# Performance work log

Measured on AMD Instinct MI355X. Metric: run time of the kernel, lower is better.

The kernel has to match this reference:

```python
import jax, jax.numpy as jnp
import numpy as np

N_NODES = 100000
N_EDGES = 1000000
D_IN = 128
D_OUT = 128
ALPHA = 0.5


def setup_inputs() -> dict:
    key = jax.random.key(0)
    k = jax.random.split(key, 8)
    x = jax.random.normal(k[0], (N_NODES, D_IN), dtype=jnp.float32)
    edge_src = jax.random.randint(k[1], (N_EDGES,), 0, N_NODES, dtype=jnp.int32)
    edge_dst = jax.random.randint(k[2], (N_EDGES,), 0, N_NODES, dtype=jnp.int32)
    s = 1.0 / np.sqrt(D_IN)
    W_sd = jax.random.uniform(k[3], (D_OUT, D_IN), jnp.float32, -s, s)
    b_sd = jax.random.uniform(k[4], (D_OUT,), jnp.float32, -s, s)
    W_ds = jax.random.uniform(k[5], (D_OUT, D_IN), jnp.float32, -s, s)
    b_ds = jax.random.uniform(k[6], (D_OUT,), jnp.float32, -s, s)
    return {"x": x, "edge_src": edge_src, "edge_dst": edge_dst,
            "W_sd": W_sd, "b_sd": b_sd, "W_ds": W_ds, "b_ds": b_ds}


def reference(x, edge_src, edge_dst, W_sd, b_sd, W_ds, b_ds):
    # adj[dst, src] = 1 for each edge.
    # adj @ x      : aggregate source features into destination rows.
    # adj.T @ x    : aggregate destination features into source rows.
    agg_sd = jax.ops.segment_sum(x[edge_src], edge_dst, num_segments=N_NODES)  # [N, D_IN]
    agg_ds = jax.ops.segment_sum(x[edge_dst], edge_src, num_segments=N_NODES)  # [N, D_IN]
    src_to_dst = agg_sd @ W_sd.T + b_sd  # torch Linear: x W^T + b
    dst_to_src = agg_ds @ W_ds.T + b_ds
    return ALPHA * src_to_dst + (1.0 - ALPHA) * dst_to_src
```

## Files before the change

kernel.cpp:

```cpp
#include <hip/hip_runtime.h>

#define NN 100000
#define NE 1000000
#define D 128
#define ALPHA 0.5f

#define OFF_W2     102400000UL
#define OFF_CNT    102531072UL
#define OFF_START  102931072UL
#define OFF_CUR    103331072UL
#define OFF_CURSOR 103731072UL
#define OFF_BUF    103731328UL
#define OFF_REC    111731328UL
#define WS_OLD     (OFF_BUF + (size_t)2 * NE * 4)
#define WS_NEW     (OFF_REC + (size_t)2 * NE * 4)

#define NB  391
#define EPB 2048

__global__ __launch_bounds__(256) void build_w2(const float* __restrict__ Wsd,
                                                const float* __restrict__ Wds,
                                                float* __restrict__ W2) {
    int idx = blockIdx.x * 256 + threadIdx.x;
    int k = idx >> 8;
    int j = idx & 255;
    float v;
    if (j < 128) v = ALPHA * Wsd[j * D + k];
    else         v = (1.0f - ALPHA) * Wds[(j - 128) * D + k];
    W2[idx] = v;
}

__global__ __launch_bounds__(256) void transform(const float* __restrict__ x,
                                                 const float* __restrict__ W2,
                                                 float* __restrict__ y) {
    __shared__ float As[64][132];
    const int tid  = threadIdx.x;
    const int brow = blockIdx.x * 64;
    const int bcol = blockIdx.y * 64;

#pragma unroll
    for (int i = 0; i < 8; ++i) {
        int f   = tid + i * 256;
        int row = f >> 5;
        int kc  = (f & 31) << 2;
        float4 g = make_float4(0.f, 0.f, 0.f, 0.f);
        int grow = brow + row;
        if (grow < NN) g = *(const float4*)&x[(size_t)grow * D + kc];
        *(float4*)&As[row][kc] = g;
    }
    __syncthreads();

    const int ty = tid >> 4;
    const int tx = tid & 15;
    float acc[4][4];
#pragma unroll
    for (int i = 0; i < 4; ++i)
#pragma unroll
        for (int j = 0; j < 4; ++j) acc[i][j] = 0.f;

#pragma unroll 2
    for (int k0 = 0; k0 < 128; k0 += 4) {
        float av[4][4], bv[4][4];
#pragma unroll
        for (int i = 0; i < 4; ++i) {
            float4 t = *(const float4*)&As[ty * 4 + i][k0];
            av[i][0] = t.x; av[i][1] = t.y; av[i][2] = t.z; av[i][3] = t.w;
        }
#pragma unroll
        for (int j = 0; j < 4; ++j) {
            float4 t = *(const float4*)&W2[(size_t)(k0 + j) * 256 + bcol + tx * 4];
            bv[j][0] = t.x; bv[j][1] = t.y; bv[j][2] = t.z; bv[j][3] = t.w;
        }
#pragma unroll
        for (int i = 0; i < 4; ++i)
#pragma unroll
            for (int c = 0; c < 4; ++c)
#pragma unroll
                for (int kk = 0; kk < 4; ++kk)
                    acc[i][c] += av[i][kk] * bv[kk][c];
    }

#pragma unroll
    for (int i = 0; i < 4; ++i) {
        int row = brow + ty * 4 + i;
        if (row < NN) {
            float4 v = make_float4(acc[i][0], acc[i][1], acc[i][2], acc[i][3]);
            *(float4*)&y[(size_t)row * 256 + bcol + tx * 4] = v;
        }
    }
}

__global__ __launch_bounds__(512) void zero_bins(int* __restrict__ binCnt) {
    int i = threadIdx.x;
    if (i < NB) binCnt[i] = 0;
}

__global__ __launch_bounds__(256) void count_bins(const int* __restrict__ esrc,
                                                  const int* __restrict__ edst,
                                                  int* __restrict__ binCnt) {
    __shared__ int h[NB];
    int t = threadIdx.x;
    for (int i = t; i < NB; i += 256) h[i] = 0;
    __syncthreads();
    int e0 = blockIdx.x * EPB;
    for (int i = t; i < EPB; i += 256) {
        int e = e0 + i;
        if (e < NE) {
            atomicAdd(&h[edst[e] >> 8], 1);
            atomicAdd(&h[esrc[e] >> 8], 1);
        }
    }
    __syncthreads();
    for (int i = t; i < NB; i += 256)
        if (h[i]) atomicAdd(&binCnt[i], h[i]);
}

__global__ __launch_bounds__(256) void scan_bins(const int* __restrict__ binCnt,
                                                 int* __restrict__ binBase,
                                                 int* __restrict__ binCursor) {
    __shared__ int v[NB];
    int t = threadIdx.x;
    for (int i = t; i < NB; i += 256) v[i] = binCnt[i];
    __syncthreads();
    if (t == 0) {
        int acc = 0;
        for (int i = 0; i < NB; ++i) { int c = v[i]; v[i] = acc; acc += c; }
    }
    __syncthreads();
    for (int i = t; i < NB; i += 256) { binBase[i] = v[i]; binCursor[i] = v[i]; }
}

__global__ __launch_bounds__(256) void place_bins(const int* __restrict__ esrc,
                                                  const int* __restrict__ edst,
                                                  int* __restrict__ binCursor,
                                                  int* __restrict__ rec4) {
    __shared__ int h[NB];
    __shared__ int base[NB];
    __shared__ int lcur[NB];
    int t = threadIdx.x;
    for (int i = t; i < NB; i += 256) h[i] = 0;
    __syncthreads();
    int e0 = blockIdx.x * EPB;
    for (int i = t; i < EPB; i += 256) {
        int e = e0 + i;
        if (e < NE) {
            atomicAdd(&h[edst[e] >> 8], 1);
            atomicAdd(&h[esrc[e] >> 8], 1);
        }
    }
    __syncthreads();
    for (int i = t; i < NB; i += 256) {
        if (h[i]) base[i] = atomicAdd(&binCursor[i], h[i]);
        lcur[i] = 0;
    }
    __syncthreads();
    for (int i = t; i < EPB; i += 256) {
        int e = e0 + i;
        if (e < NE) {
            int s = esrc[e], d = edst[e];
            int bd = d >> 8, bs = s >> 8;
            int p1 = atomicAdd(&lcur[bd], 1);
            rec4[base[bd] + p1] = ((d & 255) << 18) | (s << 1);
            int p2 = atomicAdd(&lcur[bs], 1);
            rec4[base[bs] + p2] = ((s & 255) << 18) | (d << 1) | 1;
        }
    }
}

__global__ __launch_bounds__(256) void build_csr(const int* __restrict__ rec4,
                                                 const int* __restrict__ binBase,
                                                 const int* __restrict__ binCnt,
                                                 int* __restrict__ buf,
                                                 int* __restrict__ start,
                                                 int* __restrict__ cnt_out) {
    __shared__ int hc[256];
    __shared__ int st[256];
    int b = blockIdx.x;
    int t = threadIdx.x;
    int node0 = b << 8;
    int r0 = binBase[b];
    int rn = binCnt[b];

    hc[t] = 0;
    __syncthreads();
    for (int i = t; i < rn; i += 256)
        atomicAdd(&hc[rec4[r0 + i] >> 18], 1);
    __syncthreads();
    if (t == 0) {
        int acc = 0;
        for (int i = 0; i < 256; ++i) { st[i] = acc; acc += hc[i]; }
    }
    __syncthreads();
    int n = node0 + t;
    if (n < NN) {
        start[n]   = r0 + st[t];
        cnt_out[n] = hc[t];
    }
    hc[t] = st[t];
    __syncthreads();
    for (int i = t; i < rn; i += 256) {
        int r = rec4[r0 + i];
        int pos = atomicAdd(&hc[r >> 18], 1);
        buf[r0 + pos] = (r & 0x3FFFF) << 7;
    }
}

__global__ __launch_bounds__(256) void gather(const int* __restrict__ start,
                                              const int* __restrict__ cnt,
                                              const int* __restrict__ buf,
                                              const float* __restrict__ y,
                                              const float* __restrict__ bsd,
                                              const float* __restrict__ bds,
                                              float* __restrict__ out) {
    int wave = blockIdx.x * 4 + (threadIdx.x >> 6);
    int lane = threadIdx.x & 63;
    if (wave >= NN) return;
    const int n  = wave;
    const int s0 = start[n];
    const int e0 = s0 + cnt[n];
    const int l2 = lane << 1;

    float a0 = ALPHA * bsd[l2]     + (1.0f - ALPHA) * bds[l2];
    float a1 = ALPHA * bsd[l2 + 1] + (1.0f - ALPHA) * bds[l2 + 1];

    int i = s0;
    for (; i + 4 <= e0; i += 4) {
        int v0 = buf[i], v1 = buf[i + 1], v2 = buf[i + 2], v3 = buf[i + 3];
        float2 p0 = *(const float2*)&y[(size_t)v0 + l2];
        float2 p1 = *(const float2*)&y[(size_t)v1 + l2];
        float2 p2 = *(const float2*)&y[(size_t)v2 + l2];
        float2 p3 = *(const float2*)&y[(size_t)v3 + l2];
        a0 += p0.x + p1.x + p2.x + p3.x;
        a1 += p0.y + p1.y + p2.y + p3.y;
    }
    for (; i < e0; ++i) {
        int v0 = buf[i];
        float2 p0 = *(const float2*)&y[(size_t)v0 + l2];
        a0 += p0.x;
        a1 += p0.y;
    }
    *(float2*)&out[(size_t)n * D + l2] = make_float2(a0, a1);
}

__global__ __launch_bounds__(256) void zero_cnt(int* __restrict__ cnt,
                                                int* __restrict__ cursor) {
    int i = blockIdx.x * 256 + threadIdx.x;
    if (i < NN) cnt[i] = 0;
    if (i == 0) *cursor = 0;
}

__global__ __launch_bounds__(256) void hist(const int* __restrict__ esrc,
                                            const int* __restrict__ edst,
                                            int* __restrict__ cnt) {
    int e = blockIdx.x * 256 + threadIdx.x;
    if (e < NE) {
        atomicAdd(&cnt[edst[e]], 1);
        atomicAdd(&cnt[esrc[e]], 1);
    }
}

__global__ __launch_bounds__(256) void alloc_ranges(const int* __restrict__ cnt,
                                                    int* __restrict__ start,
                                                    int* __restrict__ cur,
                                                    int* __restrict__ cursor) {
    int n    = blockIdx.x * 256 + threadIdx.x;
    int lane = threadIdx.x & 63;
    int v    = (n < NN) ? cnt[n] : 0;
    int incl = v;
#pragma unroll
    for (int off = 1; off < 64; off <<= 1) {
        int t = __shfl_up(incl, off, 64);
        if (lane >= off) incl += t;
    }
    int total = __shfl(incl, 63, 64);
    int base  = 0;
    if (lane == 63) base = atomicAdd(cursor, total);
    base = __shfl(base, 63, 64);
    if (n < NN) {
        int s = base + incl - v;
        start[n] = s;
        cur[n]   = s;
    }
}

__global__ __launch_bounds__(256) void fill(const int* __restrict__ esrc,
                                            const int* __restrict__ edst,
                                            int* __restrict__ cur,
                                            int* __restrict__ buf) {
    int e = blockIdx.x * 256 + threadIdx.x;
    if (e < NE) {
        int s = esrc[e], d = edst[e];
        int p = atomicAdd(&cur[d], 1);
        buf[p] = s * 256;
        int q = atomicAdd(&cur[s], 1);
        buf[q] = d * 256 + 128;
    }
}

__global__ __launch_bounds__(256) void init_out(const float* __restrict__ bsd,
                                                const float* __restrict__ bds,
                                                float* __restrict__ out) {
    int idx = blockIdx.x * 256 + threadIdx.x;
    int d4 = (idx & 31) << 2;
    float4 v;
    v.x = ALPHA * bsd[d4 + 0] + (1.0f - ALPHA) * bds[d4 + 0];
    v.y = ALPHA * bsd[d4 + 1] + (1.0f - ALPHA) * bds[d4 + 1];
    v.z = ALPHA * bsd[d4 + 2] + (1.0f - ALPHA) * bds[d4 + 2];
    v.w = ALPHA * bsd[d4 + 3] + (1.0f - ALPHA) * bds[d4 + 3];
    ((float4*)out)[idx] = v;
}

__global__ __launch_bounds__(256) void scatter(const int* __restrict__ esrc,
                                               const int* __restrict__ edst,
                                               const float* __restrict__ y,
                                               float* __restrict__ out) {
    const int lane = threadIdx.x & 63;
    const int wave = blockIdx.x * 4 + (threadIdx.x >> 6);
    const int nw   = gridDim.x * 4;
    const int l2   = lane << 1;
    for (int e = wave; e < NE; e += nw) {
        int s = esrc[e];
        int d = edst[e];
        float2 a = *(const float2*)&y[(size_t)s * 256 + l2];
        float2 b = *(const float2*)&y[(size_t)d * 256 + 128 + l2];
        float* od = &out[(size_t)d * D + l2];
        float* os = &out[(size_t)s * D + l2];
        unsafeAtomicAdd(od + 0, a.x);
        unsafeAtomicAdd(od + 1, a.y);
        unsafeAtomicAdd(os + 0, b.x);
        unsafeAtomicAdd(os + 1, b.y);
    }
}

extern "C" void kernel_launch(void* const* d_in, const int* in_sizes, int n_in,
                              void* d_out, int out_size, void* d_ws, size_t ws_size,
                              hipStream_t stream) {
    const float* x    = (const float*)d_in[0];
    const int*   esrc = (const int*)  d_in[1];
    const int*   edst = (const int*)  d_in[2];
    const float* Wsd  = (const float*)d_in[3];
    const float* bsd  = (const float*)d_in[4];
    const float* Wds  = (const float*)d_in[5];
    const float* bds  = (const float*)d_in[6];
    float* out = (float*)d_out;

    char* ws = (char*)d_ws;
    float* y  = (float*)ws;
    float* W2 = (float*)(ws + OFF_W2);

    build_w2<<<128, 256, 0, stream>>>(Wsd, Wds, W2);
    transform<<<dim3((NN + 63) / 64, 4), 256, 0, stream>>>(x, W2, y);

    int* cnt    = (int*)(ws + OFF_CNT);
    int* start  = (int*)(ws + OFF_START);
    int* buf    = (int*)(ws + OFF_BUF);

    if (ws_size >= WS_NEW) {
        int* binCnt    = (int*)(ws + OFF_CUR);
        int* binBase   = (int*)(ws + OFF_CUR + 4096);
        int* binCursor = (int*)(ws + OFF_CUR + 8192);
        int* rec4      = (int*)(ws + OFF_REC);
        const int nblk = (NE + EPB - 1) / EPB;
        zero_bins<<<1, 512, 0, stream>>>(binCnt);
        count_bins<<<nblk, 256, 0, stream>>>(esrc, edst, binCnt);
        scan_bins<<<1, 256, 0, stream>>>(binCnt, binBase, binCursor);
        place_bins<<<nblk, 256, 0, stream>>>(esrc, edst, binCursor, rec4);
        build_csr<<<NB, 256, 0, stream>>>(rec4, binBase, binCnt, buf, start, cnt);
        gather<<<(NN + 3) / 4, 256, 0, stream>>>(start, cnt, buf, y, bsd, bds, out);
    } else if (ws_size >= WS_OLD) {
        int* cur    = (int*)(ws + OFF_CUR);
        int* cursor = (int*)(ws + OFF_CURSOR);
        zero_cnt<<<(NN + 255) / 256, 256, 0, stream>>>(cnt, cursor);
        hist<<<(NE + 255) / 256, 256, 0, stream>>>(esrc, edst, cnt);
        alloc_ranges<<<(NN + 255) / 256, 256, 0, stream>>>(cnt, start, cur, cursor);
        fill<<<(NE + 255) / 256, 256, 0, stream>>>(esrc, edst, cur, buf);
        gather<<<(NN + 3) / 4, 256, 0, stream>>>(start, cnt, buf, y, bsd, bds, out);
    } else {
        init_out<<<(NN * D / 4) / 256, 256, 0, stream>>>(bsd, bds, out);
        scatter<<<2048, 256, 0, stream>>>(esrc, edst, y, out);
    }
}
```

Baseline: 419.1 us.

## Aggregate raw features first, then apply a fused K=256 linear transform

Swaps the order of aggregation and linear projection. Each node's incoming and outgoing neighbour features from x are gathered into a 256-wide buffer z, split by edge direction. A single GEMM with a stacked 256x128 weight and a pre-combined bias then produces the output. The gather now reads the smaller x rows instead of the 256-wide transformed y, which is meant to improve cache locality. The GEMM now reads z straight from global memory with no shared-memory staging, and the old fallback paths for smaller workspaces are removed.

```diff
diff --git a/kernel.cpp b/kernel.cpp
--- a/kernel.cpp
+++ b/kernel.cpp
@@ -6,88 +6,32 @@
 #define ALPHA 0.5f
 
 #define OFF_W2     102400000UL
-#define OFF_CNT    102531072UL
-#define OFF_START  102931072UL
-#define OFF_CUR    103331072UL
-#define OFF_CURSOR 103731072UL
-#define OFF_BUF    103731328UL
-#define OFF_REC    111731328UL
-#define WS_OLD     (OFF_BUF + (size_t)2 * NE * 4)
-#define WS_NEW     (OFF_REC + (size_t)2 * NE * 4)
+#define OFF_BIAS   102531072UL
+#define OFF_CNT    102531584UL
+#define OFF_START  102931584UL
+#define OFF_BINC   103331584UL
+#define OFF_BINB   103333632UL
+#define OFF_BINCUR 103335680UL
+#define OFF_BUF    103337728UL
+#define OFF_REC    111337728UL
 
 #define NB  391
 #define EPB 2048
 
-__global__ __launch_bounds__(256) void build_w2(const float* __restrict__ Wsd,
-                                                const float* __restrict__ Wds,
-                                                float* __restrict__ W2) {
+__global__ __launch_bounds__(256) void build_w2b(const float* __restrict__ Wsd,
+                                                 const float* __restrict__ Wds,
+                                                 const float* __restrict__ bsd,
+                                                 const float* __restrict__ bds,
+                                                 float* __restrict__ W2,
+                                                 float* __restrict__ bias) {
     int idx = blockIdx.x * 256 + threadIdx.x;
-    int k = idx >> 8;
-    int j = idx & 255;
+    int k = idx >> 7;
+    int j = idx & 127;
     float v;
-    if (j < 128) v = ALPHA * Wsd[j * D + k];
-    else         v = (1.0f - ALPHA) * Wds[(j - 128) * D + k];
+    if (k < 128) v = ALPHA * Wsd[j * D + k];
+    else         v = (1.0f - ALPHA) * Wds[j * D + (k - 128)];
     W2[idx] = v;
-}
-
-__global__ __launch_bounds__(256) void transform(const float* __restrict__ x,
-                                                 const float* __restrict__ W2,
-                                                 float* __restrict__ y) {
-    __shared__ float As[64][132];
-    const int tid  = threadIdx.x;
-    const int brow = blockIdx.x * 64;
-    const int bcol = blockIdx.y * 64;
-
-#pragma unroll
-    for (int i = 0; i < 8; ++i) {
-        int f   = tid + i * 256;
-        int row = f >> 5;
-        int kc  = (f & 31) << 2;
-        float4 g = make_float4(0.f, 0.f, 0.f, 0.f);
-        int grow = brow + row;
-        if (grow < NN) g = *(const float4*)&x[(size_t)grow * D + kc];
-        *(float4*)&As[row][kc] = g;
-    }
-    __syncthreads();
-
-    const int ty = tid >> 4;
-    const int tx = tid & 15;
-    float acc[4][4];
-#pragma unroll
-    for (int i = 0; i < 4; ++i)
-#pragma unroll
-        for (int j = 0; j < 4; ++j) acc[i][j] = 0.f;
-
-#pragma unroll 2
-    for (int k0 = 0; k0 < 128; k0 += 4) {
-        float av[4][4], bv[4][4];
-#pragma unroll
-        for (int i = 0; i < 4; ++i) {
-            float4 t = *(const float4*)&As[ty * 4 + i][k0];
-            av[i][0] = t.x; av[i][1] = t.y; av[i][2] = t.z; av[i][3] = t.w;
-        }
-#pragma unroll
-        for (int j = 0; j < 4; ++j) {
-            float4 t = *(const float4*)&W2[(size_t)(k0 + j) * 256 + bcol + tx * 4];
-            bv[j][0] = t.x; bv[j][1] = t.y; bv[j][2] = t.z; bv[j][3] = t.w;
-        }
-#pragma unroll
-        for (int i = 0; i < 4; ++i)
-#pragma unroll
-            for (int c = 0; c < 4; ++c)
-#pragma unroll
-                for (int kk = 0; kk < 4; ++kk)
-                    acc[i][c] += av[i][kk] * bv[kk][c];
-    }
-
-#pragma unroll
-    for (int i = 0; i < 4; ++i) {
-        int row = brow + ty * 4 + i;
-        if (row < NN) {
-            float4 v = make_float4(acc[i][0], acc[i][1], acc[i][2], acc[i][3]);
-            *(float4*)&y[(size_t)row * 256 + bcol + tx * 4] = v;
-        }
-    }
+    if (idx < 128) bias[idx] = ALPHA * bsd[idx] + (1.0f - ALPHA) * bds[idx];
 }
 
 __global__ __launch_bounds__(512) void zero_bins(int* __restrict__ binCnt) {
@@ -201,134 +145,108 @@
     for (int i = t; i < rn; i += 256) {
         int r = rec4[r0 + i];
         int pos = atomicAdd(&hc[r >> 18], 1);
-        buf[r0 + pos] = (r & 0x3FFFF) << 7;
-    }
-}
-
-__global__ __launch_bounds__(256) void gather(const int* __restrict__ start,
-                                              const int* __restrict__ cnt,
-                                              const int* __restrict__ buf,
-                                              const float* __restrict__ y,
-                                              const float* __restrict__ bsd,
-                                              const float* __restrict__ bds,
-                                              float* __restrict__ out) {
+        buf[r0 + pos] = r & 0x3FFFF;
+    }
+}
+
+__global__ __launch_bounds__(256) void gather_z(const int* __restrict__ start,
+                                                const int* __restrict__ cnt,
+                                                const int* __restrict__ buf,
+                                                const float* __restrict__ x,
+                                                float* __restrict__ z) {
     int wave = blockIdx.x * 4 + (threadIdx.x >> 6);
     int lane = threadIdx.x & 63;
     if (wave >= NN) return;
-    const int n  = wave;
-    const int s0 = start[n];
-    const int e0 = s0 + cnt[n];
+    const int s0 = start[wave];
+    const int e0 = s0 + cnt[wave];
     const int l2 = lane << 1;
 
-    float a0 = ALPHA * bsd[l2]     + (1.0f - ALPHA) * bds[l2];
-    float a1 = ALPHA * bsd[l2 + 1] + (1.0f - ALPHA) * bds[l2 + 1];
+    float a0 = 0.f, a1 = 0.f;
+    float b0 = 0.f, b1 = 0.f;
+
+#define ACCUM(v, p) if ((v) & 1) { b0 += (p).x; b1 += (p).y; } \
+                    else         { a0 += (p).x; a1 += (p).y; }
 
     int i = s0;
     for (; i + 4 <= e0; i += 4) {
         int v0 = buf[i], v1 = buf[i + 1], v2 = buf[i + 2], v3 = buf[i + 3];
-        float2 p0 = *(const float2*)&y[(size_t)v0 + l2];
-        float2 p1 = *(const float2*)&y[(size_t)v1 + l2];
-        float2 p2 = *(const float2*)&y[(size_t)v2 + l2];
-        float2 p3 = *(const float2*)&y[(size_t)v3 + l2];
-        a0 += p0.x + p1.x + p2.x + p3.x;
-        a1 += p0.y + p1.y + p2.y + p3.y;
+        float2 p0 = *(const float2*)&x[(size_t)(v0 >> 1) * D + l2];
+        float2 p1 = *(const float2*)&x[(size_t)(v1 >> 1) * D + l2];
+        float2 p2 = *(const float2*)&x[(size_t)(v2 >> 1) * D + l2];
+        float2 p3 = *(const float2*)&x[(size_t)(v3 >> 1) * D + l2];
+        ACCUM(v0, p0) ACCUM(v1, p1) ACCUM(v2, p2) ACCUM(v3, p3)
     }
     for (; i < e0; ++i) {
         int v0 = buf[i];
-        float2 p0 = *(const float2*)&y[(size_t)v0 + l2];
-        a0 += p0.x;
-        a1 += p0.y;
-    }
-    *(float2*)&out[(size_t)n * D + l2] = make_float2(a0, a1);
-}
-
-__global__ __launch_bounds__(256) void zero_cnt(int* __restrict__ cnt,
-                                                int* __restrict__ cursor) {
-    int i = blockIdx.x * 256 + threadIdx.x;
-    if (i < NN) cnt[i] = 0;
-    if (i == 0) *cursor = 0;
-}
-
-__global__ __launch_bounds__(256) void hist(const int* __restrict__ esrc,
-                                            const int* __restrict__ edst,
-                                            int* __restrict__ cnt) {
-    int e = blockIdx.x * 256 + threadIdx.x;
-    if (e < NE) {
-        atomicAdd(&cnt[edst[e]], 1);
-        atomicAdd(&cnt[esrc[e]], 1);
-    }
-}
-
-__global__ __launch_bounds__(256) void alloc_ranges(const int* __restrict__ cnt,
-                                                    int* __restrict__ start,
-                                                    int* __restrict__ cur,
-                                                    int* __restrict__ cursor) {
-    int n    = blockIdx.x * 256 + threadIdx.x;
-    int lane = threadIdx.x & 63;
-    int v    = (n < NN) ? cnt[n] : 0;
-    int incl = v;
-#pragma unroll
-    for (int off = 1; off < 64; off <<= 1) {
-        int t = __shfl_up(incl, off, 64);
-        if (lane >= off) incl += t;
-    }
-    int total = __shfl(incl, 63, 64);
-    int base  = 0;
-    if (lane == 63) base = atomicAdd(cursor, total);
-    base = __shfl(base, 63, 64);
-    if (n < NN) {
-        int s = base + incl - v;
-        start[n] = s;
-        cur[n]   = s;
-    }
-}
-
-__global__ __launch_bounds__(256) void fill(const int* __restrict__ esrc,
-                                            const int* __restrict__ edst,
-                                            int* __restrict__ cur,
-                                            int* __restrict__ buf) {
-    int e = blockIdx.x * 256 + threadIdx.x;
-    if (e < NE) {
-        int s = esrc[e], d = edst[e];
-        int p = atomicAdd(&cur[d], 1);
-        buf[p] = s * 256;
-        int q = atomicAdd(&cur[s], 1);
-        buf[q] = d * 256 + 128;
-    }
-}
-
-__global__ __launch_bounds__(256) void init_out(const float* __restrict__ bsd,
-                                                const float* __restrict__ bds,
-                                                float* __restrict__ out) {
-    int idx = blockIdx.x * 256 + threadIdx.x;
-    int d4 = (idx & 31) << 2;
-    float4 v;
-    v.x = ALPHA * bsd[d4 + 0] + (1.0f - ALPHA) * bds[d4 + 0];
-    v.y = ALPHA * bsd[d4 + 1] + (1.0f - ALPHA) * bds[d4 + 1];
-    v.z = ALPHA * bsd[d4 + 2] + (1.0f - ALPHA) * bds[d4 + 2];
-    v.w = ALPHA * bsd[d4 + 3] + (1.0f - ALPHA) * bds[d4 + 3];
-    ((float4*)out)[idx] = v;
-}
-
-__global__ __launch_bounds__(256) void scatter(const int* __restrict__ esrc,
-                                               const int* __restrict__ edst,
-                                               const float* __restrict__ y,
-                                               float* __restrict__ out) {
-    const int lane = threadIdx.x & 63;
-    const int wave = blockIdx.x * 4 + (threadIdx.x >> 6);
-    const int nw   = gridDim.x * 4;
-    const int l2   = lane << 1;
-    for (int e = wave; e < NE; e += nw) {
-        int s = esrc[e];
-        int d = edst[e];
-        float2 a = *(const float2*)&y[(size_t)s * 256 + l2];
-        float2 b = *(const float2*)&y[(size_t)d * 256 + 128 + l2];
-        float* od = &out[(size_t)d * D + l2];
-        float* os = &out[(size_t)s * D + l2];
-        unsafeAtomicAdd(od + 0, a.x);
-        unsafeAtomicAdd(od + 1, a.y);
-        unsafeAtomicAdd(os + 0, b.x);
-        unsafeAtomicAdd(os + 1, b.y);
+        float2 p0 = *(const float2*)&x[(size_t)(v0 >> 1) * D + l2];
+        ACCUM(v0, p0)
+    }
+#undef ACCUM
+
+    *(float2*)&z[(size_t)wave * 256 + l2]       = make_float2(a0, a1);
+    *(float2*)&z[(size_t)wave * 256 + 128 + l2] = make_float2(b0, b1);
+}
+
+__global__ __launch_bounds__(256) void transform_z(const float* __restrict__ z,
+                                                   const float* __restrict__ W2,
+                                                   const float* __restrict__ bias,
+                                                   float* __restrict__ out) {
+    const int tid  = threadIdx.x;
+    const int brow = blockIdx.x * 64;
+    const int ty   = tid >> 4;
+    const int tx   = tid & 15;
+    const int c0   = tx << 2;
+
+    float acc[4][2][4];
+#pragma unroll
+    for (int i = 0; i < 4; ++i)
+#pragma unroll
+        for (int g = 0; g < 2; ++g)
+#pragma unroll
+            for (int c = 0; c < 4; ++c) acc[i][g][c] = 0.f;
+
+    size_t zbase[4];
+    int    rvalid[4];
+#pragma unroll
+    for (int i = 0; i < 4; ++i) {
+        int row = brow + ty * 4 + i;
+        rvalid[i] = (row < NN);
+        zbase[i]  = (size_t)(rvalid[i] ? row : 0) * 256;
+    }
+
+#pragma unroll 2
+    for (int k0 = 0; k0 < 256; k0 += 4) {
+        float4 av[4];
+#pragma unroll
+        for (int i = 0; i < 4; ++i)
+            av[i] = *(const float4*)&z[zbase[i] + k0];
+#pragma unroll
+        for (int j = 0; j < 4; ++j) {
+            float4 q0 = *(const float4*)&W2[(k0 + j) * 128 + c0];
+            float4 q1 = *(const float4*)&W2[(k0 + j) * 128 + 64 + c0];
+#pragma unroll
+            for (int i = 0; i < 4; ++i) {
+                float a = (&av[i].x)[j];
+                acc[i][0][0] += a * q0.x; acc[i][0][1] += a * q0.y;
+                acc[i][0][2] += a * q0.z; acc[i][0][3] += a * q0.w;
+                acc[i][1][0] += a * q1.x; acc[i][1][1] += a * q1.y;
+                acc[i][1][2] += a * q1.z; acc[i][1][3] += a * q1.w;
+            }
+        }
+    }
+
+    float4 bb0 = *(const float4*)&bias[c0];
+    float4 bb1 = *(const float4*)&bias[64 + c0];
+#pragma unroll
+    for (int i = 0; i < 4; ++i) {
+        if (!rvalid[i]) continue;
+        int row = brow + ty * 4 + i;
+        float4 o0 = make_float4(acc[i][0][0] + bb0.x, acc[i][0][1] + bb0.y,
+                                acc[i][0][2] + bb0.z, acc[i][0][3] + bb0.w);
+        float4 o1 = make_float4(acc[i][1][0] + bb1.x, acc[i][1][1] + bb1.y,
+                                acc[i][1][2] + bb1.z, acc[i][1][3] + bb1.w);
+        *(float4*)&out[(size_t)row * D + c0]      = o0;
+        *(float4*)&out[(size_t)row * D + 64 + c0] = o1;
     }
 }
 
@@ -344,39 +262,26 @@
     const float* bds  = (const float*)d_in[6];
     float* out = (float*)d_out;
 
-    char* ws = (char*)d_ws;
-    float* y  = (float*)ws;
-    float* W2 = (float*)(ws + OFF_W2);
-
-    build_w2<<<128, 256, 0, stream>>>(Wsd, Wds, W2);
-    transform<<<dim3((NN + 63) / 64, 4), 256, 0, stream>>>(x, W2, y);
-
-    int* cnt    = (int*)(ws + OFF_CNT);
-    int* start  = (int*)(ws + OFF_START);
-    int* buf    = (int*)(ws + OFF_BUF);
-
-    if (ws_size >= WS_NEW) {
-        int* binCnt    = (int*)(ws + OFF_CUR);
-        int* binBase   = (int*)(ws + OFF_CUR + 4096);
-        int* binCursor = (int*)(ws + OFF_CUR + 8192);
-        int* rec4      = (int*)(ws + OFF_REC);
-        const int nblk = (NE + EPB - 1) / EPB;
-        zero_bins<<<1, 512, 0, stream>>>(binCnt);
-        count_bins<<<nblk, 256, 0, stream>>>(esrc, edst, binCnt);
-        scan_bins<<<1, 256, 0, stream>>>(binCnt, binBase, binCursor);
-        place_bins<<<nblk, 256, 0, stream>>>(esrc, edst, binCursor, rec4);
-        build_csr<<<NB, 256, 0, stream>>>(rec4, binBase, binCnt, buf, start, cnt);
-        gather<<<(NN + 3) / 4, 256, 0, stream>>>(start, cnt, buf, y, bsd, bds, out);
-    } else if (ws_size >= WS_OLD) {
-        int* cur    = (int*)(ws + OFF_CUR);
-        int* cursor = (int*)(ws + OFF_CURSOR);
-        zero_cnt<<<(NN + 255) / 256, 256, 0, stream>>>(cnt, cursor);
-        hist<<<(NE + 255) / 256, 256, 0, stream>>>(esrc, edst, cnt);
-        alloc_ranges<<<(NN + 255) / 256, 256, 0, stream>>>(cnt, start, cur, cursor);
-        fill<<<(NE + 255) / 256, 256, 0, stream>>>(esrc, edst, cur, buf);
-        gather<<<(NN + 3) / 4, 256, 0, stream>>>(start, cnt, buf, y, bsd, bds, out);
-    } else {
-        init_out<<<(NN * D / 4) / 256, 256, 0, stream>>>(bsd, bds, out);
-        scatter<<<2048, 256, 0, stream>>>(esrc, edst, y, out);
-    }
-}
+    char*  ws       = (char*)d_ws;
+    float* z        = (float*)ws;
+    float* W2       = (float*)(ws + OFF_W2);
+    float* bias     = (float*)(ws + OFF_BIAS);
+    int*   cnt      = (int*)(ws + OFF_CNT);
+    int*   start    = (int*)(ws + OFF_START);
+    int*   binCnt   = (int*)(ws + OFF_BINC);
+    int*   binBase  = (int*)(ws + OFF_BINB);
+    int*   binCursor= (int*)(ws + OFF_BINCUR);
+    int*   buf      = (int*)(ws + OFF_BUF);
+    int*   rec4     = (int*)(ws + OFF_REC);
+
+    const int nblk = (NE + EPB - 1) / EPB;
+
+    build_w2b<<<128, 256, 0, stream>>>(Wsd, Wds, bsd, bds, W2, bias);
+    zero_bins<<<1, 512, 0, stream>>>(binCnt);
+    count_bins<<<nblk, 256, 0, stream>>>(esrc, edst, binCnt);
+    scan_bins<<<1, 256, 0, stream>>>(binCnt, binBase, binCursor);
+    place_bins<<<nblk, 256, 0, stream>>>(esrc, edst, binCursor, rec4);
+    build_csr<<<NB, 256, 0, stream>>>(rec4, binBase, binCnt, buf, start, cnt);
+    gather_z<<<(NN + 3) / 4, 256, 0, stream>>>(start, cnt, buf, x, z);
+    transform_z<<<(NN + 63) / 64, 256, 0, stream>>>(z, W2, bias, out);
+}
```

Result: slower. 473.1 us (+12.9%).
